# Kernel tuning notes

Measured on AMD Instinct MI355X. Metric: run time of the kernel, lower is better.

The kernel has to match this reference:

```python
import jax, jax.numpy as jnp
import numpy as np


def _patch_size(w):
    # mirrors PatchLoss size selection (static shape -> Python branch is fine)
    if w == 512:
        return 64
    elif 256 <= w < 512:
        return 32
    raise ValueError('error size')


def setup_inputs() -> dict:
    key = jax.random.key(0)
    k1, k2 = jax.random.split(key)
    shape = (1, 3, 32, 512, 512)  # (b=1, c, t, h, w)
    x = jax.random.normal(k1, shape, dtype=jnp.float32)
    x_r = jax.random.normal(k2, shape, dtype=jnp.float32)
    return {"x": x, "x_r": x_r}


def reference(x, x_r):
    _, c, t, h, w = x.shape
    size = _patch_size(w)
    tc, hc, wc = 1, size // 2, size // 2
    # L = |(x+1)/2 - (x_r+1)/2| ; original detaches before pooling
    L = jnp.abs((x + 1.0) / 2.0 - (x_r + 1.0) / 2.0)
    D = jax.lax.stop_gradient(L)[0]  # (c, t, h, w), batch squeezed
    # patch means over (c, hc, wc) for each frame (tc=1) and spatial block
    nh, nw = h // hc, w // wc
    P = D.reshape(c, t, nh, hc, nw, wc).mean(axis=(0, 3, 5))  # (t, nh, nw)
    # max over spatial patches; original init max_patch=0.0, so clamp at 0
    max_patches = jnp.maximum(P.max(axis=(1, 2)), 0.0)  # (t,)
    return jnp.log(max_patches.mean())
```

## Files before the change

### kernel.cpp

```cpp
#include <hip/hip_runtime.h>
#include <math.h>


#define NPART 8192

__global__ __launch_bounds__(256) void patch_sum_kernel(
    const float* __restrict__ x, const float* __restrict__ xr,
    float* __restrict__ part) {
  const int b  = blockIdx.x;
  const int tid = threadIdx.x;
  const size_t base = ((size_t)(b >> 4) * 512 + (size_t)(b & 15) * 32) * 512;
  const float4* __restrict__ a4 = (const float4*)(x  + base);
  const float4* __restrict__ b4 = (const float4*)(xr + base);

  float acc = 0.f;
#pragma unroll 8
  for (int i = 0; i < 16; ++i) {
    float4 a = a4[i * 256 + tid];
    float4 c = b4[i * 256 + tid];
    acc += fabsf(a.x - c.x) + fabsf(a.y - c.y)
         + fabsf(a.z - c.z) + fabsf(a.w - c.w);
  }

  __shared__ float s[16];
  if (tid < 16) s[tid] = 0.f;
  __syncthreads();
  acc += __shfl_down(acc, 4, 8);
  acc += __shfl_down(acc, 2, 8);
  acc += __shfl_down(acc, 1, 8);
  if ((tid & 7) == 0) atomicAdd(&s[(tid & 127) >> 3], acc);
  __syncthreads();
  if (tid < 16) part[(size_t)b * 16 + tid] = s[tid];
}

__global__ __launch_bounds__(1024) void finalize_kernel(
    const float* __restrict__ part, float* __restrict__ out) {
  const int tid = threadIdx.x;
  const int t = tid >> 5;
  const int j = tid & 31;
  float m = -1e30f;
#pragma unroll
  for (int k = 0; k < 8; ++k) {
    int p = t * 256 + j + 32 * k;
    float v = part[p] + part[NPART + p] + part[2 * NPART + p];
    m = fmaxf(m, v);
  }
#pragma unroll
  for (int o = 16; o > 0; o >>= 1) m = fmaxf(m, __shfl_down(m, o, 32));
  __shared__ float s[32];
  if (j == 0) s[t] = fmaxf(m * (0.5f / 3072.0f), 0.f);
  __syncthreads();
  if (tid < 32) {
    float v = s[tid];
#pragma unroll
    for (int o = 16; o > 0; o >>= 1) v += __shfl_down(v, o, 32);
    if (tid == 0) out[0] = logf(v * (1.0f / 32.0f));
  }
}

extern "C" void kernel_launch(void* const* d_in, const int* in_sizes, int n_in,
                              void* d_out, int out_size, void* d_ws, size_t ws_size,
                              hipStream_t stream) {
  const float* x  = (const float*)d_in[0];
  const float* xr = (const float*)d_in[1];
  float* part = (float*)d_ws;
  float* out  = (float*)d_out;

  patch_sum_kernel<<<1536, 256, 0, stream>>>(x, xr, part);
  finalize_kernel<<<1, 1024, 0, stream>>>(part, out);
}
```

Before: 215.4 us.

## Split patch-sum blocks into half-row tiles with batched loads and no atomics

```diff
diff --git a/kernel.cpp b/kernel.cpp
--- a/kernel.cpp
+++ b/kernel.cpp
@@ -7,30 +7,54 @@
 __global__ __launch_bounds__(256) void patch_sum_kernel(
     const float* __restrict__ x, const float* __restrict__ xr,
     float* __restrict__ part) {
-  const int b  = blockIdx.x;
+  const int b   = blockIdx.x;
   const int tid = threadIdx.x;
-  const size_t base = ((size_t)(b >> 4) * 512 + (size_t)(b & 15) * 32) * 512;
-  const float4* __restrict__ a4 = (const float4*)(x  + base);
-  const float4* __restrict__ b4 = (const float4*)(xr + base);
+  const int ch   = b >> 10;
+  const int rem  = b & 1023;
+  const int t    = rem >> 5;
+  const int sub  = rem & 31;
+  const int ph   = sub >> 1;
+  const int half = sub & 1;
+  const size_t base4 = ((size_t)(ch * 32 + t) * 512 + (size_t)ph * 32) * 128
+                     + (size_t)half * 64;
+  const float4* __restrict__ a4 = (const float4*)x  + base4;
+  const float4* __restrict__ b4 = (const float4*)xr + base4;
 
-  float acc = 0.f;
-#pragma unroll 8
-  for (int i = 0; i < 16; ++i) {
-    float4 a = a4[i * 256 + tid];
-    float4 c = b4[i * 256 + tid];
-    acc += fabsf(a.x - c.x) + fabsf(a.y - c.y)
-         + fabsf(a.z - c.z) + fabsf(a.w - c.w);
+  float4 a[8], c[8];
+#pragma unroll
+  for (int i = 0; i < 8; ++i) {
+    int idx = i * 256 + tid;
+    a[i] = a4[(size_t)(idx >> 6) * 128 + (idx & 63)];
+  }
+#pragma unroll
+  for (int i = 0; i < 8; ++i) {
+    int idx = i * 256 + tid;
+    c[i] = b4[(size_t)(idx >> 6) * 128 + (idx & 63)];
   }
 
-  __shared__ float s[16];
-  if (tid < 16) s[tid] = 0.f;
-  __syncthreads();
+  float s0 = 0.f, s1 = 0.f, s2 = 0.f, s3 = 0.f;
+#pragma unroll
+  for (int i = 0; i < 8; ++i) {
+    s0 += fabsf(a[i].x - c[i].x);
+    s1 += fabsf(a[i].y - c[i].y);
+    s2 += fabsf(a[i].z - c[i].z);
+    s3 += fabsf(a[i].w - c[i].w);
+  }
+  float acc = (s0 + s1) + (s2 + s3);
+
   acc += __shfl_down(acc, 4, 8);
   acc += __shfl_down(acc, 2, 8);
   acc += __shfl_down(acc, 1, 8);
-  if ((tid & 7) == 0) atomicAdd(&s[(tid & 127) >> 3], acc);
+  __shared__ float s[32];
+  if ((tid & 7) == 0) {
+    int m = tid >> 3;
+    s[(m >> 3) * 8 + (m & 7)] = acc;
+  }
   __syncthreads();
-  if (tid < 16) part[(size_t)b * 16 + tid] = s[tid];
+  if (tid < 8) {
+    float v = (s[tid] + s[8 + tid]) + (s[16 + tid] + s[24 + tid]);
+    part[(size_t)ch * 8192 + t * 256 + ph * 16 + half * 8 + tid] = v;
+  }
 }
 
 __global__ __launch_bounds__(1024) void finalize_kernel(
@@ -66,6 +90,6 @@
   float* part = (float*)d_ws;
   float* out  = (float*)d_out;
 
-  patch_sum_kernel<<<1536, 256, 0, stream>>>(x, xr, part);
+  patch_sum_kernel<<<3072, 256, 0, stream>>>(x, xr, part);
   finalize_kernel<<<1, 1024, 0, stream>>>(part, out);
 }
```

Result: faster. 209.8 us (-2.6%).
